# Performance work log

Measured on AMD Instinct MI355X. Metric: run time of the kernel, lower is better.

The kernel has to match this reference:

```python
import jax, jax.numpy as jnp
import numpy as np

N, D, HID, G, E2 = 2048, 256, 128, 8, 16384


def _mlp(h, w1, b1, g, be, w2, b2):
    # Linear -> ReLU -> BatchNorm1d (training mode, biased batch var) -> Linear
    h = jax.nn.relu(h @ w1 + b1)
    mu = h.mean(axis=0)
    var = ((h - mu) ** 2).mean(axis=0)
    h = (h - mu) / jnp.sqrt(var + 1e-5) * g + be
    return h @ w2 + b2


def setup_inputs() -> dict:
    key = jax.random.key(0)
    ks = jax.random.split(key, 12)
    x = jax.random.normal(ks[0], (N, D), jnp.float32)
    src = jax.random.randint(ks[1], (E2,), 0, N)
    dst = jax.random.randint(ks[2], (E2,), 0, N)
    src = jnp.where(src == dst, (src + 1) % N, src)  # no self loops
    edge_index = jnp.stack([jnp.concatenate([src, dst]),
                            jnp.concatenate([dst, src])])  # symmetric
    batch = jnp.sort(jax.random.randint(ks[3], (N,), 0, G))
    def lin(k, i, o):
        return 0.1 * jax.random.normal(k, (i, o), jnp.float32)
    out = dict(x=x, edge_index=edge_index, batch=batch)
    dims = [(1, HID, HID), (HID, HID, HID), (HID, HID, 1)]
    names = [("w11", "b11", "g1", "be1", "w12", "b12"),
             ("w21", "b21", "g2", "be2", "w22", "b22"),
             ("w31", "b31", "g3", "be3", "w32", "b32")]
    k = 4
    for (i, h, o), n in zip(dims, names):
        out[n[0]] = lin(ks[k], i, h)
        out[n[1]] = jnp.zeros((h,), jnp.float32)
        out[n[2]] = jnp.ones((h,), jnp.float32)
        out[n[3]] = jnp.zeros((h,), jnp.float32)
        out[n[4]] = lin(ks[k + 1], h, o)
        out[n[5]] = jnp.zeros((o,), jnp.float32)
        k += 2
    return out


def reference(x, edge_index, batch,
              w11, b11, g1, be1, w12, b12,
              w21, b21, g2, be2, w22, b22,
              w31, b31, g3, be3, w32, b32):
    n = x.shape[0]
    # dense adjacency from edge_index; L = D - A (unnormalized graph Laplacian)
    A = jnp.zeros((n, n), x.dtype).at[edge_index[0], edge_index[1]].set(1.0)
    deg = A.sum(axis=1)
    # entropy term: V = x*(Lx) - x*(Ax) + A(x*x), Lx = deg*x - Ax
    Ax = A @ x
    V = x * (deg[:, None] * x - Ax) - x * Ax + A @ (x * x)
    V = jnp.linalg.norm(V, axis=1)  # [n]
    # per-graph softmax over the batch segments
    mx = jax.ops.segment_max(V, batch, num_segments=G)
    ex = jnp.exp(V - mx[batch])
    P = ex / jax.ops.segment_sum(ex, batch, num_segments=G)[batch]
    P = jnp.where(P == 0.0, 1.0, P)
    ent = -P * jnp.log(P)  # [n]

    # GINConv (eps=0): mlp(x + sum_{j in N(i)} x_j) = mlp(x + A @ x)
    def gin(h, w1, b1, g, be, w2, b2):
        return _mlp(h + A @ h, w1, b1, g, be, w2, b2)

    h = gin(ent[:, None], w11, b11, g1, be1, w12, b12)
    h = gin(h, w21, b21, g2, be2, w22, b22)
    h = gin(h, w31, b31, g3, be3, w32, b32)
    p = jax.nn.sigmoid(h[:, 0])  # [n] node probabilities

    gamma = ent.sum()
    loss = gamma - jnp.vdot(ent, p) + jnp.vdot(p, A @ p)

    # greedy conditional expectation (sequential MIS-style selection)
    order = jnp.argsort(-p)

    def step(carry, idx):
        dummy, sel, rej = carry
        nb = A[idx] > 0.0  # neighbor mask [n]
        deg0 = ~jnp.any(nb)
        sel = sel.at[idx].set(sel[idx] | deg0)  # isolated node -> selected
        eligible = (~rej[idx]) & (~sel[idx])
        s = jnp.where(nb, 0.0, dummy).at[idx].set(1.0)
        li = gamma - jnp.vdot(ent, s) + jnp.vdot(s, A @ s)
        accept = eligible & (li <= loss)
        sel = sel.at[idx].set(sel[idx] | accept)
        rej = rej | (nb & accept)
        dummy = jnp.where(accept, s, dummy)
        return (dummy, sel, rej), None

    init = (p, jnp.zeros(n, dtype=bool), jnp.zeros(n, dtype=bool))
    (dummy, sel, rej), _ = jax.lax.scan(step, init, order)

    # graph reconstruction (masked instead of compacted, for static shapes)
    mask = sel.astype(x.dtype)
    x_pooled = x * mask[:, None]
    A2 = A @ A
    A3 = A2 @ A
    eye = jnp.eye(n, dtype=x.dtype)
    adj_pooled = (1.0 - eye) * jnp.clip(A2 + A3, 0.0, 1.0) * (mask[:, None] * mask[None, :])
    batch_pooled = jnp.where(sel, batch, -1)
    return x_pooled, adj_pooled, sel, batch_pooled, loss
```

## Files before the change

### kernel.cpp

```cpp
#include <hip/hip_runtime.h>
#include <math.h>

#define NN 2048
#define DIMF 256
#define HIDN 128
#define NG 8
#define NEDGES 32768
#define W32 32
#define TRI_CAP 131072
#define TRI_LDS 4864

typedef unsigned long long u64;
typedef unsigned char u8;
typedef unsigned short u16;

__global__ void k_init(u64* __restrict__ rowbits, int* __restrict__ segstart) {
  int i = blockIdx.x * blockDim.x + threadIdx.x;
  for (int k = i; k < NN * W32; k += gridDim.x * blockDim.x) rowbits[k] = 0ull;
  if (i <= NG) segstart[i] = NN;
}

__global__ void k_edges(const int* __restrict__ ei, u64* __restrict__ rowbits) {
  int e = blockIdx.x * blockDim.x + threadIdx.x;
  if (e >= NEDGES) return;
  int u = ei[e], v = ei[NEDGES + e];
  atomicOr(&rowbits[((size_t)u << 5) + (v >> 6)], 1ull << (v & 63));
}

__global__ void k_deg(const u64* __restrict__ rowbits, int* __restrict__ deg,
                      const int* __restrict__ batch, int* __restrict__ segstart) {
  int i = blockIdx.x * blockDim.x + threadIdx.x;
  if (i >= NN) return;
  int c = 0;
  for (int w = 0; w < W32; ++w) c += __popcll(rowbits[(i << 5) + w]);
  deg[i] = c;
  if (i == 0 || batch[i] != batch[i - 1]) segstart[batch[i]] = i;
}

__global__ void k_scan2048(const int* __restrict__ in, int* __restrict__ out) {
  __shared__ int part[256];
  int t = threadIdx.x;
  int v[8]; int s = 0;
  for (int k = 0; k < 8; ++k) { v[k] = in[t * 8 + k]; s += v[k]; }
  part[t] = s;
  __syncthreads();
  for (int off = 1; off < 256; off <<= 1) {
    int y = (t >= off) ? part[t - off] : 0;
    __syncthreads();
    part[t] += y;
    __syncthreads();
  }
  int run = part[t] - s;
  for (int k = 0; k < 8; ++k) { out[t * 8 + k] = run; run += v[k]; }
  if (t == 255) out[NN] = part[255];
}

__global__ void k_extract(const u64* __restrict__ rowbits, const int* __restrict__ rp,
                          int* __restrict__ col, int* __restrict__ cnt) {
  int i = blockIdx.x * blockDim.x + threadIdx.x;
  if (i >= NN) return;
  const u64* ri = rowbits + ((size_t)i << 5);
  int o = rp[i];
  for (int w = 0; w < W32; ++w) {
    u64 b = ri[w];
    while (b) { col[o++] = (w << 6) + __builtin_ctzll(b); b &= b - 1; }
  }
  int c = 0;
  for (int e = rp[i]; e < o; ++e) {
    const u64* ra = rowbits + ((size_t)col[e] << 5);
    for (int w = 0; w < W32; ++w) c += __popcll(ra[w] & ri[w]);
  }
  cnt[i] = c;
}

__global__ void k_trifill(const u64* __restrict__ rowbits, const int* __restrict__ rp,
                          const int* __restrict__ col, const int* __restrict__ tp,
                          int2* __restrict__ tri) {
  int i = blockIdx.x * blockDim.x + threadIdx.x;
  if (i >= NN) return;
  const u64* ri = rowbits + ((size_t)i << 5);
  int o = tp[i];
  for (int e = rp[i]; e < rp[i + 1]; ++e) {
    int a = col[e];
    const u64* ra = rowbits + ((size_t)a << 5);
    for (int w = 0; w < W32; ++w) {
      u64 b = ra[w] & ri[w];
      while (b) {
        int j = (w << 6) + __builtin_ctzll(b);
        if (o < TRI_CAP) tri[o] = make_int2(a, j);
        ++o;
        b &= b - 1;
      }
    }
  }
}

__global__ void k_V(const float* __restrict__ x, const int* __restrict__ rp,
                    const int* __restrict__ col, float* __restrict__ V) {
  int i = blockIdx.x; int t = threadIdx.x;
  float xi = x[i * DIMF + t];
  float s1 = 0.f, s2 = 0.f;
  int r0 = rp[i], r1 = rp[i + 1];
  for (int e = r0; e < r1; ++e) {
    float xj = x[col[e] * DIMF + t];
    s1 += xj; s2 += xj * xj;
  }
  float dg = (float)(r1 - r0);
  float val = dg * xi * xi - 2.f * xi * s1 + s2;
  __shared__ double red[DIMF];
  red[t] = (double)val * (double)val;
  __syncthreads();
  for (int off = DIMF / 2; off > 0; off >>= 1) { if (t < off) red[t] += red[t + off]; __syncthreads(); }
  if (t == 0) V[i] = (float)sqrt(red[0]);
}

__global__ void k_soft(const float* __restrict__ V, const int* __restrict__ segstart,
                       float* __restrict__ ent, double* __restrict__ seggamma) {
  int g = blockIdx.x; int t = threadIdx.x;
  int s = segstart[g];
  int e = NN;
  for (int gg = g + 1; gg <= NG; ++gg) { int v = segstart[gg]; if (v < e) e = v; }
  if (s >= e) { if (t == 0) seggamma[g] = 0.0; return; }
  __shared__ float fm[256];
  __shared__ double dd[256];
  float m = -3.0e38f;
  for (int i = s + t; i < e; i += 256) m = fmaxf(m, V[i]);
  fm[t] = m; __syncthreads();
  for (int off = 128; off > 0; off >>= 1) { if (t < off) fm[t] = fmaxf(fm[t], fm[t + off]); __syncthreads(); }
  float mx = fm[0];
  __syncthreads();
  double sum = 0.0;
  for (int i = s + t; i < e; i += 256) sum += exp((double)V[i] - (double)mx);
  dd[t] = sum; __syncthreads();
  for (int off = 128; off > 0; off >>= 1) { if (t < off) dd[t] += dd[t + off]; __syncthreads(); }
  double tot = dd[0];
  __syncthreads();
  double gs = 0.0;
  for (int i = s + t; i < e; i += 256) {
    double P = exp((double)V[i] - (double)mx) / tot;
    float ev = (P > 0.0) ? (float)(-P * log(P)) : 0.f;
    ent[i] = ev;
    gs += (double)ev;
  }
  dd[t] = gs; __syncthreads();
  for (int off = 128; off > 0; off >>= 1) { if (t < off) dd[t] += dd[t + off]; __syncthreads(); }
  if (t == 0) seggamma[g] = dd[0];
}

__global__ void k_agg1(const float* __restrict__ ent, const int* __restrict__ rp,
                       const int* __restrict__ col, float* __restrict__ agg) {
  int i = blockIdx.x * blockDim.x + threadIdx.x;
  if (i >= NN) return;
  float a = ent[i];
  for (int e = rp[i]; e < rp[i + 1]; ++e) a += ent[col[e]];
  agg[i] = a;
}

__global__ void k_lin1(const float* __restrict__ agg, const float* __restrict__ w,
                       const float* __restrict__ b, float* __restrict__ t) {
  int idx = blockIdx.x * blockDim.x + threadIdx.x;
  if (idx >= NN * HIDN) return;
  int i = idx >> 7, k = idx & 127;
  float v = agg[i] * w[k] + b[k];
  t[idx] = v > 0.f ? v : 0.f;
}

__global__ void k_bn(const float* __restrict__ t, const float* __restrict__ g,
                     const float* __restrict__ be, float* __restrict__ scale,
                     float* __restrict__ shift) {
  int k = blockIdx.x; int tid = threadIdx.x;
  __shared__ double red[256];
  double s = 0.0;
  for (int i = tid; i < NN; i += 256) s += (double)t[i * HIDN + k];
  red[tid] = s; __syncthreads();
  for (int off = 128; off > 0; off >>= 1) { if (tid < off) red[tid] += red[tid + off]; __syncthreads(); }
  double mu = red[0] / NN;
  __syncthreads();
  double v = 0.0;
  for (int i = tid; i < NN; i += 256) { double dv = (double)t[i * HIDN + k] - mu; v += dv * dv; }
  red[tid] = v; __syncthreads();
  for (int off = 128; off > 0; off >>= 1) { if (tid < off) red[tid] += red[tid + off]; __syncthreads(); }
  if (tid == 0) {
    float var = (float)(red[0] / NN);
    float sc = g[k] / sqrtf(var + 1e-5f);
    scale[k] = sc;
    shift[k] = be[k] - (float)mu * sc;
  }
}

template<int PRE, int RELU>
__global__ void k_mm(const float* __restrict__ in, const float* __restrict__ Wm,
                     const float* __restrict__ bias, const float* __restrict__ scale,
                     const float* __restrict__ shift, float* __restrict__ out) {
  __shared__ float ti[8][HIDN];
  int r0 = blockIdx.x * 8; int t = threadIdx.x;
  for (int r = 0; r < 8; ++r) {
    float v = in[(r0 + r) * HIDN + t];
    if (PRE) v = v * scale[t] + shift[t];
    ti[r][t] = v;
  }
  __syncthreads();
  float acc[8];
  #pragma unroll
  for (int r = 0; r < 8; ++r) acc[r] = 0.f;
  for (int k = 0; k < HIDN; ++k) {
    float w = Wm[k * HIDN + t];
    #pragma unroll
    for (int r = 0; r < 8; ++r) acc[r] += ti[r][k] * w;
  }
  for (int r = 0; r < 8; ++r) {
    float v = acc[r] + bias[t];
    if (RELU) v = fmaxf(v, 0.f);
    out[(r0 + r) * HIDN + t] = v;
  }
}

__global__ void k_agg128(const float* __restrict__ h, const int* __restrict__ rp,
                         const int* __restrict__ col, float* __restrict__ agg) {
  int i = blockIdx.x; int t = threadIdx.x;
  float a = h[i * HIDN + t];
  for (int e = rp[i]; e < rp[i + 1]; ++e) a += h[col[e] * HIDN + t];
  agg[i * HIDN + t] = a;
}

__global__ void k_lin3(const float* __restrict__ tn, const float* __restrict__ scale,
                       const float* __restrict__ shift, const float* __restrict__ w32,
                       const float* __restrict__ b32, float* __restrict__ p) {
  int i = blockIdx.x; int t = threadIdx.x;
  float v = (tn[i * HIDN + t] * scale[t] + shift[t]) * w32[t];
  __shared__ float red[HIDN];
  red[t] = v; __syncthreads();
  for (int off = 64; off > 0; off >>= 1) { if (t < off) red[t] += red[t + off]; __syncthreads(); }
  if (t == 0) {
    float h3 = red[0] + b32[0];
    p[i] = 1.f / (1.f + expf(-h3));
  }
}

__global__ void k_q0(const float* __restrict__ p, const float* __restrict__ ent,
                     const int* __restrict__ rp, const int* __restrict__ col,
                     float* __restrict__ q0, float* __restrict__ e0) {
  int i = blockIdx.x * blockDim.x + threadIdx.x;
  if (i >= NN) return;
  float s = 0.f, es = 0.f;
  for (int e = rp[i]; e < rp[i + 1]; ++e) {
    int j = col[e];
    float pj = p[j];
    s += pj; es += ent[j] * pj;
  }
  q0[i] = s; e0[i] = es;
}

__global__ void k_loss(const float* __restrict__ ent, const float* __restrict__ p,
                       const float* __restrict__ q0, const double* __restrict__ seggamma,
                       double* __restrict__ scal) {
  __shared__ double ra[256], rb[256];
  int t = threadIdx.x;
  double a = 0.0, b = 0.0;
  for (int i = t; i < NN; i += 256) { a += (double)ent[i] * (double)p[i]; b += (double)p[i] * (double)q0[i]; }
  ra[t] = a; rb[t] = b; __syncthreads();
  for (int off = 128; off > 0; off >>= 1) {
    if (t < off) { ra[t] += ra[t + off]; rb[t] += rb[t + off]; }
    __syncthreads();
  }
  if (t == 0) {
    double gamma = 0.0;
    for (int g = 0; g < NG; ++g) gamma += seggamma[g];
    scal[0] = gamma; scal[1] = ra[0]; scal[2] = rb[0];
    scal[3] = gamma - ra[0] + rb[0];
  }
}

__global__ void k_sort(const float* __restrict__ p, int* __restrict__ order) {
  __shared__ u64 s[NN];
  int t = threadIdx.x;
  for (int k = t; k < NN; k += 1024) {
    unsigned b = __float_as_uint(p[k]);
    unsigned ss = (b & 0x80000000u) ? ~b : (b | 0x80000000u);
    s[k] = ((u64)(~ss) << 32) | (unsigned)k;
  }
  __syncthreads();
  for (int k = 2; k <= NN; k <<= 1) {
    for (int j = k >> 1; j > 0; j >>= 1) {
      for (int i = t; i < NN; i += 1024) {
        int ixj = i ^ j;
        if (ixj > i) {
          bool up = ((i & k) == 0);
          u64 a = s[i], b = s[ixj];
          if ((a > b) == up) { s[i] = b; s[ixj] = a; }
        }
      }
      __syncthreads();
    }
  }
  order[t] = (int)(s[t] & 0xFFFFFFFFull);
  order[t + 1024] = (int)(s[t + 1024] & 0xFFFFFFFFull);
}

#define DPP2(ctrl)                                                                        \
  a += __int_as_float(__builtin_amdgcn_update_dpp(0, __float_as_int(a), ctrl, 0xf, 0xf, true)); \
  b += __int_as_float(__builtin_amdgcn_update_dpp(0, __float_as_int(b), ctrl, 0xf, 0xf, true));

__device__ __forceinline__ void red2(float& a, float& b) {
  DPP2(0x111)
  DPP2(0x112)
  DPP2(0x114)
  DPP2(0x118)
  DPP2(0x142)
  DPP2(0x143)
  a = __int_as_float(__builtin_amdgcn_readlane(__float_as_int(a), 63));
  b = __int_as_float(__builtin_amdgcn_readlane(__float_as_int(b), 63));
}

__global__ void __launch_bounds__(1024, 1) k_greedy(
    const int* __restrict__ rp, const int* __restrict__ col,
    const int* __restrict__ tp, const int2* __restrict__ tri,
    const int* __restrict__ order, const float* __restrict__ p,
    const float* __restrict__ ent, const float* __restrict__ q0,
    const float* __restrict__ e0, const double* __restrict__ scal,
    u8* __restrict__ selb_g) {
  __shared__ float2 dq[NN];
  __shared__ float2 ee[NN];
  __shared__ u16 colL[NEDGES];
  __shared__ u16 ordl[NN];
  __shared__ uint2 rtP[NN + 1];
  __shared__ ushort2 triL[TRI_LDS];
  __shared__ unsigned decidedL[64], selL[64];
  __shared__ unsigned maskL[2];
  __shared__ float4 svA[2][16];
  int t = threadIdx.x;
  int w = t >> 6, lane = t & 63;

  for (int i = t; i < NN; i += 1024) {
    dq[i] = make_float2(p[i], q0[i]);
    ee[i] = make_float2(ent[i], e0[i]);
    ordl[i] = (u16)order[i];
    int tv0 = tp[i]; if (tv0 > 65535) tv0 = 65535;
    int tv1 = tp[i + 1]; if (tv1 > 65535) tv1 = 65535;
    rtP[i] = make_uint2((unsigned)rp[i] | ((unsigned)tv0 << 16),
                        (unsigned)rp[i + 1] | ((unsigned)tv1 << 16));
  }
  for (int i = t; i < NEDGES; i += 1024) colL[i] = (u16)col[i];
  for (int i = t; i < TRI_LDS; i += 1024) {
    int2 ab = tri[i];
    triL[i] = make_ushort2((u16)(ab.x & 2047), (u16)(ab.y & 2047));
  }
  if (t < 64) { decidedL[t] = 0u; selL[t] = 0u; }
  if (t < 2) maskL[t] = 0u;
  double gamma = scal[0], loss = scal[3];
  double ed = scal[1], dAd = scal[2];
  __syncthreads();
  for (int i = t; i < NN; i += 1024) {
    if (((rtP[i].y & 0xffffu) - (rtP[i].x & 0xffffu)) == 0u) {
      atomicOr(&decidedL[i >> 5], 1u << (i & 31));
      atomicOr(&selL[i >> 5], 1u << (i & 31));
    }
  }
  __syncthreads();

  int pos = 0, rc = 0;
  while (pos < NN) {
    int b = rc & 1; ++rc;
    int step = pos + w;
    if (step < NN) {
      int idx = ordl[step];
      if (!((decidedL[idx >> 5] >> (idx & 31)) & 1u)) {
        uint2 rt = rtP[idx];
        int r0 = rt.x & 0xffff, r1 = rt.y & 0xffff;
        int t0 = rt.x >> 16, t1 = rt.y >> 16;
        float2 dqi = dq[idx];
        float2 eei = ee[idx];
        float s2 = 0.f, st = 0.f;
        for (int e = r0 + lane; e < r1; e += 64) {
          float2 v = dq[colL[e]];
          s2 -= v.y * v.x;
        }
        if (t1 <= TRI_LDS) {
          for (int e = t0 + lane; e < t1; e += 64) {
            ushort2 ab = triL[e];
            st += dq[ab.x].x * dq[ab.y].x;
          }
        } else {
          int g0 = tp[idx], g1 = tp[idx + 1];
          if (g0 > TRI_CAP) g0 = TRI_CAP;
          if (g1 > TRI_CAP) g1 = TRI_CAP;
          for (int e = g0 + lane; e < g1; e += 64) {
            int2 ab = tri[e];
            st += dq[ab.x].x * dq[ab.y].x;
          }
        }
        red2(s2, st);
        float d0 = 1.f - dqi.x;
        float S1 = -eei.y + eei.x * d0;
        float S2 = s2 + dqi.y * d0;
        float sn = -dqi.y;
        double cross = 2.0 * (double)d0 * (double)sn + (double)st;
        double li = gamma - (ed + (double)S1) + (dAd + 2.0 * (double)S2 + cross);
        if (li <= loss && lane == 0) {
          svA[b][w] = make_float4(S1, S2, d0, st);
          atomicOr(&maskL[b], 1u << w);
        }
      }
    }
    __syncthreads();
    unsigned mask = maskL[b];
    if (mask == 0u) { pos += 16; continue; }
    int k = __builtin_ctz(mask);
    int idx = ordl[pos + k];
    float4 A = svA[b][k];
    float2 dqi = dq[idx];
    uint2 rt = rtP[idx];
    int r0 = rt.x & 0xffff, r1 = rt.y & 0xffff;
    {
      double cross = 2.0 * (double)A.z * (double)(-dqi.y) + (double)A.w;
      ed += (double)A.x;
      dAd += 2.0 * (double)A.y + cross;
    }
    __syncthreads();
    if (t == 0) maskL[b] = 0u;
    for (int e = r0 + w; e < r1; e += 16) {
      int a = colL[e];
      float da = -dq[a].x;
      if (da != 0.f) {
        float ea = ee[a].x;
        uint2 art = rtP[a];
        int b0 = art.x & 0xffff, b1 = art.y & 0xffff;
        for (int eb = b0 + lane; eb < b1; eb += 64) {
          int bb = colL[eb];
          atomicAdd(&dq[bb].y, da);
          atomicAdd(&ee[bb].y, ea * da);
        }
      }
    }
    {
      float ei = ee[idx].x;
      for (int e = r0 + t; e < r1; e += 1024) {
        int bb = colL[e];
        atomicAdd(&dq[bb].y, A.z);
        atomicAdd(&ee[bb].y, ei * A.z);
      }
    }
    __syncthreads();
    if (t == 0) {
      dq[idx].x = 1.f;
      atomicOr(&decidedL[idx >> 5], 1u << (idx & 31));
      atomicOr(&selL[idx >> 5], 1u << (idx & 31));
    }
    for (int e = r0 + t; e < r1; e += 1024) {
      int j = colL[e];
      dq[j].x = 0.f;
      atomicOr(&decidedL[j >> 5], 1u << (j & 31));
    }
    __syncthreads();
    pos += k + 1;
  }
  for (int i = t; i < NN; i += 1024)
    selb_g[i] = (u8)((selL[i >> 5] >> (i & 31)) & 1u);
}

__global__ void k_reach(const u64* __restrict__ src, const int* __restrict__ rp,
                        const int* __restrict__ col, u64* __restrict__ dst) {
  int node = blockIdx.x * 2 + (threadIdx.x >> 5);
  int w = threadIdx.x & 31;
  u64 acc = 0;
  for (int e = rp[node]; e < rp[node + 1]; ++e) acc |= src[((size_t)col[e] << 5) + w];
  dst[((size_t)node << 5) + w] = acc;
}

__global__ void k_out(const u64* __restrict__ row2, const u64* __restrict__ row3,
                      const u8* __restrict__ selb, const float* __restrict__ x,
                      const int* __restrict__ batch, const double* __restrict__ scal,
                      float* __restrict__ o_x, float* __restrict__ o_adj,
                      float* __restrict__ o_sel, float* __restrict__ o_bat,
                      float* __restrict__ o_loss) {
  int idx = blockIdx.x * blockDim.x + threadIdx.x;
  {
    int i = idx >> 11, j = idx & 2047;
    int wo = (i << 5) + (j >> 6);
    u64 b = (row2[wo] | row3[wo]) >> (j & 63);
    o_adj[idx] = ((b & 1ull) && i != j && selb[i] && selb[j]) ? 1.f : 0.f;
  }
  if (idx < NN * DIMF) {
    int i = idx >> 8;
    o_x[idx] = selb[i] ? x[idx] : 0.f;
  }
  if (idx < NN) {
    o_sel[idx] = selb[idx] ? 1.f : 0.f;
    o_bat[idx] = selb[idx] ? (float)batch[idx] : -1.f;
  }
  if (idx == 0) o_loss[0] = (float)scal[3];
}

extern "C" void kernel_launch(void* const* d_in, const int* in_sizes, int n_in,
                              void* d_out, int out_size, void* d_ws, size_t ws_size,
                              hipStream_t stream) {
  const float* x    = (const float*)d_in[0];
  const int*   ei   = (const int*)d_in[1];
  const int*   batch= (const int*)d_in[2];
  const float* w11  = (const float*)d_in[3];
  const float* b11  = (const float*)d_in[4];
  const float* g1   = (const float*)d_in[5];
  const float* be1  = (const float*)d_in[6];
  const float* w12  = (const float*)d_in[7];
  const float* b12  = (const float*)d_in[8];
  const float* w21  = (const float*)d_in[9];
  const float* b21  = (const float*)d_in[10];
  const float* g2   = (const float*)d_in[11];
  const float* be2  = (const float*)d_in[12];
  const float* w22  = (const float*)d_in[13];
  const float* b22  = (const float*)d_in[14];
  const float* w31  = (const float*)d_in[15];
  const float* b31  = (const float*)d_in[16];
  const float* g3   = (const float*)d_in[17];
  const float* be3  = (const float*)d_in[18];
  const float* w32  = (const float*)d_in[19];
  const float* b32  = (const float*)d_in[20];

  char* wsb = (char*)d_ws;
  size_t cur = 0;
  auto alloc = [&](size_t bytes) -> void* {
    void* pp = wsb + cur;
    cur += (bytes + 255) & ~(size_t)255;
    return pp;
  };
  u64*    rowbits = (u64*)alloc((size_t)NN * W32 * 8);
  u64*    row2    = (u64*)alloc((size_t)NN * W32 * 8);
  u64*    row3    = (u64*)alloc((size_t)NN * W32 * 8);
  double* seggam  = (double*)alloc(NG * 8);
  double* scal    = (double*)alloc(4 * 8);
  int*    deg     = (int*)alloc(NN * 4);
  int*    rowptr  = (int*)alloc((NN + 1) * 4);
  int*    colx    = (int*)alloc(65536 * 4);
  int*    tricnt  = (int*)alloc(NN * 4);
  int*    triptr  = (int*)alloc((NN + 1) * 4);
  int2*   tri     = (int2*)alloc((size_t)TRI_CAP * 8);
  int*    segst   = (int*)alloc((NG + 1) * 4);
  int*    order   = (int*)alloc(NN * 4);
  float*  ent     = (float*)alloc(NN * 4);
  float*  V       = (float*)alloc(NN * 4);
  float*  p       = (float*)alloc(NN * 4);
  float*  q0      = (float*)alloc(NN * 4);
  float*  e0      = (float*)alloc(NN * 4);
  float*  agg1    = (float*)alloc(NN * 4);
  float*  scale   = (float*)alloc(HIDN * 4);
  float*  shift   = (float*)alloc(HIDN * 4);
  float*  tA      = (float*)alloc((size_t)NN * HIDN * 4);
  float*  tB      = (float*)alloc((size_t)NN * HIDN * 4);
  float*  tC      = (float*)alloc((size_t)NN * HIDN * 4);
  u8*     selb    = (u8*)alloc(NN);

  float* out    = (float*)d_out;
  float* o_x    = out;
  float* o_adj  = out + 524288;
  float* o_sel  = out + 4718592;
  float* o_bat  = out + 4720640;
  float* o_loss = out + 4722688;

  k_init<<<64, 256, 0, stream>>>(rowbits, segst);
  k_edges<<<128, 256, 0, stream>>>(ei, rowbits);
  k_deg<<<8, 256, 0, stream>>>(rowbits, deg, batch, segst);
  k_scan2048<<<1, 256, 0, stream>>>(deg, rowptr);
  k_extract<<<8, 256, 0, stream>>>(rowbits, rowptr, colx, tricnt);
  k_scan2048<<<1, 256, 0, stream>>>(tricnt, triptr);
  k_trifill<<<8, 256, 0, stream>>>(rowbits, rowptr, colx, triptr, tri);
  k_V<<<NN, 256, 0, stream>>>(x, rowptr, colx, V);
  k_soft<<<NG, 256, 0, stream>>>(V, segst, ent, seggam);

  k_agg1<<<8, 256, 0, stream>>>(ent, rowptr, colx, agg1);
  k_lin1<<<1024, 256, 0, stream>>>(agg1, w11, b11, tA);
  k_bn<<<HIDN, 256, 0, stream>>>(tA, g1, be1, scale, shift);
  k_mm<1, 0><<<NN / 8, HIDN, 0, stream>>>(tA, w12, b12, scale, shift, tB);
  k_agg128<<<NN, HIDN, 0, stream>>>(tB, rowptr, colx, tC);
  k_mm<0, 1><<<NN / 8, HIDN, 0, stream>>>(tC, w21, b21, scale, shift, tA);
  k_bn<<<HIDN, 256, 0, stream>>>(tA, g2, be2, scale, shift);
  k_mm<1, 0><<<NN / 8, HIDN, 0, stream>>>(tA, w22, b22, scale, shift, tB);
  k_agg128<<<NN, HIDN, 0, stream>>>(tB, rowptr, colx, tC);
  k_mm<0, 1><<<NN / 8, HIDN, 0, stream>>>(tC, w31, b31, scale, shift, tA);
  k_bn<<<HIDN, 256, 0, stream>>>(tA, g3, be3, scale, shift);
  k_lin3<<<NN, HIDN, 0, stream>>>(tA, scale, shift, w32, b32, p);

  k_q0<<<8, 256, 0, stream>>>(p, ent, rowptr, colx, q0, e0);
  k_loss<<<1, 256, 0, stream>>>(ent, p, q0, seggam, scal);
  k_sort<<<1, 1024, 0, stream>>>(p, order);
  k_greedy<<<1, 1024, 0, stream>>>(rowptr, colx, triptr, tri, order, p, ent, q0, e0, scal, selb);

  k_reach<<<NN / 2, 64, 0, stream>>>(rowbits, rowptr, colx, row2);
  k_reach<<<NN / 2, 64, 0, stream>>>(row2, rowptr, colx, row3);
  k_out<<<NN * NN / 256, 256, 0, stream>>>(row2, row3, selb, x, batch, scal,
                                           o_x, o_adj, o_sel, o_bat, o_loss);

  (void)in_sizes; (void)n_in; (void)out_size; (void)ws_size;
}
```

Baseline: 1.132 ms.

## Fuse preprocessing and MLP stages into one cooperative persistent kernel

Measured after the change: 1.863 ms. +64.6%, slower.

```diff
diff --git a/kernel.cpp b/kernel.cpp
--- a/kernel.cpp
+++ b/kernel.cpp
@@ -1,5 +1,8 @@
 #include <hip/hip_runtime.h>
+#include <hip/hip_cooperative_groups.h>
 #include <math.h>
+
+namespace cg = cooperative_groups;
 
 #define NN 2048
 #define DIMF 256
@@ -9,293 +12,345 @@
 #define W32 32
 #define TRI_CAP 131072
 #define TRI_LDS 4864
+#define NB 64
+#define NT 1024
+#define GSZ (NB * NT)
 
 typedef unsigned long long u64;
 typedef unsigned char u8;
 typedef unsigned short u16;
 
-__global__ void k_init(u64* __restrict__ rowbits, int* __restrict__ segstart) {
-  int i = blockIdx.x * blockDim.x + threadIdx.x;
-  for (int k = i; k < NN * W32; k += gridDim.x * blockDim.x) rowbits[k] = 0ull;
-  if (i <= NG) segstart[i] = NN;
-}
-
-__global__ void k_edges(const int* __restrict__ ei, u64* __restrict__ rowbits) {
-  int e = blockIdx.x * blockDim.x + threadIdx.x;
-  if (e >= NEDGES) return;
-  int u = ei[e], v = ei[NEDGES + e];
-  atomicOr(&rowbits[((size_t)u << 5) + (v >> 6)], 1ull << (v & 63));
-}
-
-__global__ void k_deg(const u64* __restrict__ rowbits, int* __restrict__ deg,
-                      const int* __restrict__ batch, int* __restrict__ segstart) {
-  int i = blockIdx.x * blockDim.x + threadIdx.x;
-  if (i >= NN) return;
-  int c = 0;
-  for (int w = 0; w < W32; ++w) c += __popcll(rowbits[(i << 5) + w]);
-  deg[i] = c;
-  if (i == 0 || batch[i] != batch[i - 1]) segstart[batch[i]] = i;
-}
-
-__global__ void k_scan2048(const int* __restrict__ in, int* __restrict__ out) {
-  __shared__ int part[256];
-  int t = threadIdx.x;
-  int v[8]; int s = 0;
-  for (int k = 0; k < 8; ++k) { v[k] = in[t * 8 + k]; s += v[k]; }
+struct Params {
+  const float* x; const int* ei; const int* batch;
+  const float* w11; const float* b11; const float* g1; const float* be1;
+  const float* w12; const float* b12;
+  const float* w21; const float* b21; const float* g2; const float* be2;
+  const float* w22; const float* b22;
+  const float* w31; const float* b31; const float* g3; const float* be3;
+  const float* w32; const float* b32;
+  u64* rowbits; u64* row2; u64* row3;
+  int* deg; int* rowptr; int* colx; int* tricnt; int* triptr; int2* tri;
+  int* segst; float* V; float* ent; double* seggam; double* lossAB; double* scal;
+  float* agg1; float* scaleS; float* shiftS;
+  float* tA; float* tB; float* tC;
+  float* p; float* q0; float* e0; int* order;
+};
+
+__device__ void scan2048b(const int* in, int* out, int* part, int t) {
+  int v0 = in[2 * t], v1 = in[2 * t + 1];
+  int s = v0 + v1;
   part[t] = s;
   __syncthreads();
-  for (int off = 1; off < 256; off <<= 1) {
+  for (int off = 1; off < 1024; off <<= 1) {
     int y = (t >= off) ? part[t - off] : 0;
     __syncthreads();
     part[t] += y;
     __syncthreads();
   }
   int run = part[t] - s;
-  for (int k = 0; k < 8; ++k) { out[t * 8 + k] = run; run += v[k]; }
-  if (t == 255) out[NN] = part[255];
-}
-
-__global__ void k_extract(const u64* __restrict__ rowbits, const int* __restrict__ rp,
-                          int* __restrict__ col, int* __restrict__ cnt) {
-  int i = blockIdx.x * blockDim.x + threadIdx.x;
-  if (i >= NN) return;
-  const u64* ri = rowbits + ((size_t)i << 5);
-  int o = rp[i];
-  for (int w = 0; w < W32; ++w) {
-    u64 b = ri[w];
-    while (b) { col[o++] = (w << 6) + __builtin_ctzll(b); b &= b - 1; }
-  }
-  int c = 0;
-  for (int e = rp[i]; e < o; ++e) {
-    const u64* ra = rowbits + ((size_t)col[e] << 5);
-    for (int w = 0; w < W32; ++w) c += __popcll(ra[w] & ri[w]);
-  }
-  cnt[i] = c;
-}
-
-__global__ void k_trifill(const u64* __restrict__ rowbits, const int* __restrict__ rp,
-                          const int* __restrict__ col, const int* __restrict__ tp,
-                          int2* __restrict__ tri) {
-  int i = blockIdx.x * blockDim.x + threadIdx.x;
-  if (i >= NN) return;
-  const u64* ri = rowbits + ((size_t)i << 5);
-  int o = tp[i];
-  for (int e = rp[i]; e < rp[i + 1]; ++e) {
-    int a = col[e];
-    const u64* ra = rowbits + ((size_t)a << 5);
-    for (int w = 0; w < W32; ++w) {
-      u64 b = ra[w] & ri[w];
-      while (b) {
-        int j = (w << 6) + __builtin_ctzll(b);
-        if (o < TRI_CAP) tri[o] = make_int2(a, j);
-        ++o;
-        b &= b - 1;
-      }
-    }
-  }
-}
-
-__global__ void k_V(const float* __restrict__ x, const int* __restrict__ rp,
-                    const int* __restrict__ col, float* __restrict__ V) {
-  int i = blockIdx.x; int t = threadIdx.x;
-  float xi = x[i * DIMF + t];
-  float s1 = 0.f, s2 = 0.f;
-  int r0 = rp[i], r1 = rp[i + 1];
-  for (int e = r0; e < r1; ++e) {
-    float xj = x[col[e] * DIMF + t];
-    s1 += xj; s2 += xj * xj;
-  }
-  float dg = (float)(r1 - r0);
-  float val = dg * xi * xi - 2.f * xi * s1 + s2;
-  __shared__ double red[DIMF];
-  red[t] = (double)val * (double)val;
-  __syncthreads();
-  for (int off = DIMF / 2; off > 0; off >>= 1) { if (t < off) red[t] += red[t + off]; __syncthreads(); }
-  if (t == 0) V[i] = (float)sqrt(red[0]);
-}
-
-__global__ void k_soft(const float* __restrict__ V, const int* __restrict__ segstart,
-                       float* __restrict__ ent, double* __restrict__ seggamma) {
-  int g = blockIdx.x; int t = threadIdx.x;
-  int s = segstart[g];
+  out[2 * t] = run; out[2 * t + 1] = run + v0;
+  if (t == 1023) out[NN] = part[1023];
+}
+
+__device__ void bn_phase(int blk, int t, int mode, const float* aggv,
+                         const float* w1, const float* b1, const float* src,
+                         const float* g, const float* be,
+                         float* scaleS, float* shiftS, double* bnP) {
+  int c = 2 * blk + (t >> 9);
+  int tid = t & 511;
+  double s = 0.0, ss = 0.0;
+  for (int r = 0; r < 4; ++r) {
+    int i = tid + 512 * r;
+    float v;
+    if (mode == 0) { v = aggv[i] * w1[c] + b1[c]; v = v > 0.f ? v : 0.f; }
+    else v = src[i * HIDN + c];
+    s += (double)v; ss += (double)v * (double)v;
+  }
+  for (int off = 32; off; off >>= 1) { s += __shfl_down(s, off); ss += __shfl_down(ss, off); }
+  int w = t >> 6;
+  if ((t & 63) == 0) { bnP[2 * w] = s; bnP[2 * w + 1] = ss; }
+  __syncthreads();
+  if (t == 0 || t == 512) {
+    int wb = (t >> 9) * 8;
+    double S = 0.0, SS = 0.0;
+    for (int k = 0; k < 8; ++k) { S += bnP[2 * (wb + k)]; SS += bnP[2 * (wb + k) + 1]; }
+    double mu = S / NN;
+    float var = (float)(SS / NN - mu * mu);
+    float sc = g[c] / sqrtf(var + 1e-5f);
+    scaleS[c] = sc;
+    shiftS[c] = be[c] - (float)mu * sc;
+  }
+  __syncthreads();
+}
+
+__device__ void mm_phase(int blk, int t, int mode, const float* aggv,
+                         const float* w1, const float* b1, const float* src,
+                         const float* scaleS, const float* shiftS,
+                         const float* W, const float* bias, int relu, float* dst,
+                         float* Wl, float* tile) {
+  int r0 = blk * 32;
+  for (int i = t; i < HIDN * HIDN; i += NT) Wl[i] = W[i];
+  for (int i = t; i < 32 * HIDN; i += NT) {
+    int r = i >> 7, k = i & 127;
+    float v;
+    if (mode == 0) { v = aggv[r0 + r] * w1[k] + b1[k]; v = v > 0.f ? v : 0.f; v = v * scaleS[k] + shiftS[k]; }
+    else if (mode == 1) v = src[(r0 + r) * HIDN + k];
+    else v = src[(r0 + r) * HIDN + k] * scaleS[k] + shiftS[k];
+    tile[i] = v;
+  }
+  __syncthreads();
+  int g = t >> 7;
+  int c = t & 127;
+  float a0 = 0.f, a1 = 0.f, a2 = 0.f, a3 = 0.f;
+  for (int k = 0; k < HIDN; ++k) {
+    float wv = Wl[k * HIDN + c];
+    a0 += tile[g * HIDN + k] * wv;
+    a1 += tile[(g + 8) * HIDN + k] * wv;
+    a2 += tile[(g + 16) * HIDN + k] * wv;
+    a3 += tile[(g + 24) * HIDN + k] * wv;
+  }
+  float bv = bias[c];
+  a0 += bv; a1 += bv; a2 += bv; a3 += bv;
+  if (relu) { a0 = fmaxf(a0, 0.f); a1 = fmaxf(a1, 0.f); a2 = fmaxf(a2, 0.f); a3 = fmaxf(a3, 0.f); }
+  dst[(r0 + g) * HIDN + c] = a0;
+  dst[(r0 + g + 8) * HIDN + c] = a1;
+  dst[(r0 + g + 16) * HIDN + c] = a2;
+  dst[(r0 + g + 24) * HIDN + c] = a3;
+  __syncthreads();
+}
+
+__device__ void soft_phase(int g, int t, const float* V, const int* segst,
+                           float* ent, double* seggam, float* fmS, double* ddS) {
+  int s = segst[g];
   int e = NN;
-  for (int gg = g + 1; gg <= NG; ++gg) { int v = segstart[gg]; if (v < e) e = v; }
-  if (s >= e) { if (t == 0) seggamma[g] = 0.0; return; }
-  __shared__ float fm[256];
-  __shared__ double dd[256];
+  for (int gg = g + 1; gg <= NG; ++gg) { int v = segst[gg]; if (v < e) e = v; }
+  if (s >= e) { if (t == 0) seggam[g] = 0.0; return; }
   float m = -3.0e38f;
-  for (int i = s + t; i < e; i += 256) m = fmaxf(m, V[i]);
-  fm[t] = m; __syncthreads();
-  for (int off = 128; off > 0; off >>= 1) { if (t < off) fm[t] = fmaxf(fm[t], fm[t + off]); __syncthreads(); }
-  float mx = fm[0];
+  for (int i = s + t; i < e; i += NT) m = fmaxf(m, V[i]);
+  fmS[t] = m; __syncthreads();
+  for (int off = 512; off; off >>= 1) { if (t < off) fmS[t] = fmaxf(fmS[t], fmS[t + off]); __syncthreads(); }
+  float mx = fmS[0];
   __syncthreads();
   double sum = 0.0;
-  for (int i = s + t; i < e; i += 256) sum += exp((double)V[i] - (double)mx);
-  dd[t] = sum; __syncthreads();
-  for (int off = 128; off > 0; off >>= 1) { if (t < off) dd[t] += dd[t + off]; __syncthreads(); }
-  double tot = dd[0];
+  for (int i = s + t; i < e; i += NT) sum += exp((double)V[i] - (double)mx);
+  ddS[t] = sum; __syncthreads();
+  for (int off = 512; off; off >>= 1) { if (t < off) ddS[t] += ddS[t + off]; __syncthreads(); }
+  double tot = ddS[0];
   __syncthreads();
   double gs = 0.0;
-  for (int i = s + t; i < e; i += 256) {
+  for (int i = s + t; i < e; i += NT) {
     double P = exp((double)V[i] - (double)mx) / tot;
     float ev = (P > 0.0) ? (float)(-P * log(P)) : 0.f;
     ent[i] = ev;
     gs += (double)ev;
   }
-  dd[t] = gs; __syncthreads();
-  for (int off = 128; off > 0; off >>= 1) { if (t < off) dd[t] += dd[t + off]; __syncthreads(); }
-  if (t == 0) seggamma[g] = dd[0];
-}
-
-__global__ void k_agg1(const float* __restrict__ ent, const int* __restrict__ rp,
-                       const int* __restrict__ col, float* __restrict__ agg) {
-  int i = blockIdx.x * blockDim.x + threadIdx.x;
-  if (i >= NN) return;
-  float a = ent[i];
-  for (int e = rp[i]; e < rp[i + 1]; ++e) a += ent[col[e]];
-  agg[i] = a;
-}
-
-__global__ void k_lin1(const float* __restrict__ agg, const float* __restrict__ w,
-                       const float* __restrict__ b, float* __restrict__ t) {
-  int idx = blockIdx.x * blockDim.x + threadIdx.x;
-  if (idx >= NN * HIDN) return;
-  int i = idx >> 7, k = idx & 127;
-  float v = agg[i] * w[k] + b[k];
-  t[idx] = v > 0.f ? v : 0.f;
-}
-
-__global__ void k_bn(const float* __restrict__ t, const float* __restrict__ g,
-                     const float* __restrict__ be, float* __restrict__ scale,
-                     float* __restrict__ shift) {
-  int k = blockIdx.x; int tid = threadIdx.x;
-  __shared__ double red[256];
-  double s = 0.0;
-  for (int i = tid; i < NN; i += 256) s += (double)t[i * HIDN + k];
-  red[tid] = s; __syncthreads();
-  for (int off = 128; off > 0; off >>= 1) { if (tid < off) red[tid] += red[tid + off]; __syncthreads(); }
-  double mu = red[0] / NN;
-  __syncthreads();
-  double v = 0.0;
-  for (int i = tid; i < NN; i += 256) { double dv = (double)t[i * HIDN + k] - mu; v += dv * dv; }
-  red[tid] = v; __syncthreads();
-  for (int off = 128; off > 0; off >>= 1) { if (tid < off) red[tid] += red[tid + off]; __syncthreads(); }
-  if (tid == 0) {
-    float var = (float)(red[0] / NN);
-    float sc = g[k] / sqrtf(var + 1e-5f);
-    scale[k] = sc;
-    shift[k] = be[k] - (float)mu * sc;
-  }
-}
-
-template<int PRE, int RELU>
-__global__ void k_mm(const float* __restrict__ in, const float* __restrict__ Wm,
-                     const float* __restrict__ bias, const float* __restrict__ scale,
-                     const float* __restrict__ shift, float* __restrict__ out) {
-  __shared__ float ti[8][HIDN];
-  int r0 = blockIdx.x * 8; int t = threadIdx.x;
-  for (int r = 0; r < 8; ++r) {
-    float v = in[(r0 + r) * HIDN + t];
-    if (PRE) v = v * scale[t] + shift[t];
-    ti[r][t] = v;
-  }
-  __syncthreads();
-  float acc[8];
-  #pragma unroll
-  for (int r = 0; r < 8; ++r) acc[r] = 0.f;
-  for (int k = 0; k < HIDN; ++k) {
-    float w = Wm[k * HIDN + t];
-    #pragma unroll
-    for (int r = 0; r < 8; ++r) acc[r] += ti[r][k] * w;
-  }
-  for (int r = 0; r < 8; ++r) {
-    float v = acc[r] + bias[t];
-    if (RELU) v = fmaxf(v, 0.f);
-    out[(r0 + r) * HIDN + t] = v;
-  }
-}
-
-__global__ void k_agg128(const float* __restrict__ h, const int* __restrict__ rp,
-                         const int* __restrict__ col, float* __restrict__ agg) {
-  int i = blockIdx.x; int t = threadIdx.x;
-  float a = h[i * HIDN + t];
-  for (int e = rp[i]; e < rp[i + 1]; ++e) a += h[col[e] * HIDN + t];
-  agg[i * HIDN + t] = a;
-}
-
-__global__ void k_lin3(const float* __restrict__ tn, const float* __restrict__ scale,
-                       const float* __restrict__ shift, const float* __restrict__ w32,
-                       const float* __restrict__ b32, float* __restrict__ p) {
-  int i = blockIdx.x; int t = threadIdx.x;
-  float v = (tn[i * HIDN + t] * scale[t] + shift[t]) * w32[t];
-  __shared__ float red[HIDN];
-  red[t] = v; __syncthreads();
-  for (int off = 64; off > 0; off >>= 1) { if (t < off) red[t] += red[t + off]; __syncthreads(); }
-  if (t == 0) {
-    float h3 = red[0] + b32[0];
-    p[i] = 1.f / (1.f + expf(-h3));
-  }
-}
-
-__global__ void k_q0(const float* __restrict__ p, const float* __restrict__ ent,
-                     const int* __restrict__ rp, const int* __restrict__ col,
-                     float* __restrict__ q0, float* __restrict__ e0) {
-  int i = blockIdx.x * blockDim.x + threadIdx.x;
-  if (i >= NN) return;
-  float s = 0.f, es = 0.f;
-  for (int e = rp[i]; e < rp[i + 1]; ++e) {
-    int j = col[e];
-    float pj = p[j];
-    s += pj; es += ent[j] * pj;
-  }
-  q0[i] = s; e0[i] = es;
-}
-
-__global__ void k_loss(const float* __restrict__ ent, const float* __restrict__ p,
-                       const float* __restrict__ q0, const double* __restrict__ seggamma,
-                       double* __restrict__ scal) {
-  __shared__ double ra[256], rb[256];
-  int t = threadIdx.x;
-  double a = 0.0, b = 0.0;
-  for (int i = t; i < NN; i += 256) { a += (double)ent[i] * (double)p[i]; b += (double)p[i] * (double)q0[i]; }
-  ra[t] = a; rb[t] = b; __syncthreads();
-  for (int off = 128; off > 0; off >>= 1) {
-    if (t < off) { ra[t] += ra[t + off]; rb[t] += rb[t + off]; }
-    __syncthreads();
-  }
-  if (t == 0) {
-    double gamma = 0.0;
-    for (int g = 0; g < NG; ++g) gamma += seggamma[g];
-    scal[0] = gamma; scal[1] = ra[0]; scal[2] = rb[0];
-    scal[3] = gamma - ra[0] + rb[0];
-  }
-}
-
-__global__ void k_sort(const float* __restrict__ p, int* __restrict__ order) {
-  __shared__ u64 s[NN];
-  int t = threadIdx.x;
-  for (int k = t; k < NN; k += 1024) {
-    unsigned b = __float_as_uint(p[k]);
-    unsigned ss = (b & 0x80000000u) ? ~b : (b | 0x80000000u);
-    s[k] = ((u64)(~ss) << 32) | (unsigned)k;
-  }
-  __syncthreads();
-  for (int k = 2; k <= NN; k <<= 1) {
-    for (int j = k >> 1; j > 0; j >>= 1) {
-      for (int i = t; i < NN; i += 1024) {
-        int ixj = i ^ j;
-        if (ixj > i) {
-          bool up = ((i & k) == 0);
-          u64 a = s[i], b = s[ixj];
-          if ((a > b) == up) { s[i] = b; s[ixj] = a; }
+  ddS[t] = gs; __syncthreads();
+  for (int off = 512; off; off >>= 1) { if (t < off) ddS[t] += ddS[t + off]; __syncthreads(); }
+  if (t == 0) seggam[g] = ddS[0];
+}
+
+__global__ void __launch_bounds__(1024, 1) mega(Params P) {
+  cg::grid_group grid = cg::this_grid();
+  int t = threadIdx.x, blk = blockIdx.x;
+  int gtid = blk * NT + t;
+
+  __shared__ double SMd[11776];
+  char* SM = (char*)SMd;
+  float* Wl = (float*)SM;
+  float* tile = (float*)(SM + 65536);
+  u64* skey = (u64*)SM;
+  int* scanP = (int*)(SM + 81920);
+  float* fmS = (float*)(SM + 81920);
+  double* ddS = (double*)(SM + 86016);
+  double* bnP = (double*)(SM + 81920);
+
+  for (int i = gtid; i < NN * W32; i += GSZ) P.rowbits[i] = 0ull;
+  if (gtid <= NG) P.segst[gtid] = NN;
+  if (gtid < 2) P.lossAB[gtid] = 0.0;
+  grid.sync();
+  for (int e = gtid; e < NEDGES; e += GSZ) {
+    int u = P.ei[e], v = P.ei[NEDGES + e];
+    atomicOr(&P.rowbits[((size_t)u << 5) + (v >> 6)], 1ull << (v & 63));
+  }
+  grid.sync();
+  if (gtid < NN) {
+    int c = 0;
+    for (int w = 0; w < W32; ++w) c += __popcll(P.rowbits[(gtid << 5) + w]);
+    P.deg[gtid] = c;
+    if (gtid == 0 || P.batch[gtid] != P.batch[gtid - 1]) P.segst[P.batch[gtid]] = gtid;
+  }
+  grid.sync();
+  if (blk == 0) scan2048b(P.deg, P.rowptr, scanP, t);
+  grid.sync();
+  if (gtid < NN) {
+    const u64* ri = P.rowbits + ((size_t)gtid << 5);
+    int o = P.rowptr[gtid];
+    for (int w = 0; w < W32; ++w) {
+      u64 b = ri[w];
+      while (b) { P.colx[o++] = (w << 6) + __builtin_ctzll(b); b &= b - 1; }
+    }
+    int c = 0;
+    for (int e = P.rowptr[gtid]; e < o; ++e) {
+      const u64* ra = P.rowbits + ((size_t)P.colx[e] << 5);
+      for (int w = 0; w < W32; ++w) c += __popcll(ra[w] & ri[w]);
+    }
+    P.tricnt[gtid] = c;
+  }
+  grid.sync();
+  if (blk == 0) scan2048b(P.tricnt, P.triptr, scanP, t);
+  grid.sync();
+  if (gtid < NN) {
+    const u64* ri = P.rowbits + ((size_t)gtid << 5);
+    int o = P.triptr[gtid];
+    for (int e = P.rowptr[gtid]; e < P.rowptr[gtid + 1]; ++e) {
+      int a = P.colx[e];
+      const u64* ra = P.rowbits + ((size_t)a << 5);
+      for (int w = 0; w < W32; ++w) {
+        u64 b = ra[w] & ri[w];
+        while (b) {
+          int j = (w << 6) + __builtin_ctzll(b);
+          if (o < TRI_CAP) P.tri[o] = make_int2(a, j);
+          ++o;
+          b &= b - 1;
         }
       }
-      __syncthreads();
-    }
-  }
-  order[t] = (int)(s[t] & 0xFFFFFFFFull);
-  order[t + 1024] = (int)(s[t + 1024] & 0xFFFFFFFFull);
-}
+    }
+  }
+  for (int i2 = gtid; i2 < NN * W32; i2 += GSZ) {
+    int node = i2 >> 5, w = i2 & 31;
+    u64 acc = 0;
+    for (int e = P.rowptr[node]; e < P.rowptr[node + 1]; ++e)
+      acc |= P.rowbits[((size_t)P.colx[e] << 5) + w];
+    P.row2[i2] = acc;
+  }
+  grid.sync();
+  for (int i2 = gtid; i2 < NN * W32; i2 += GSZ) {
+    int node = i2 >> 5, w = i2 & 31;
+    u64 acc = 0;
+    for (int e = P.rowptr[node]; e < P.rowptr[node + 1]; ++e)
+      acc |= P.row2[((size_t)P.colx[e] << 5) + w];
+    P.row3[i2] = acc;
+  }
+  grid.sync();
+  {
+    int node = gtid >> 5, lane = gtid & 31;
+    int r0 = P.rowptr[node], r1 = P.rowptr[node + 1];
+    double acc = 0.0;
+    for (int r = 0; r < 8; ++r) {
+      int d = lane + 32 * r;
+      float xi = P.x[node * DIMF + d];
+      float s1 = 0.f, s2 = 0.f;
+      for (int e = r0; e < r1; ++e) {
+        float xj = P.x[P.colx[e] * DIMF + d];
+        s1 += xj; s2 += xj * xj;
+      }
+      float dg = (float)(r1 - r0);
+      float val = dg * xi * xi - 2.f * xi * s1 + s2;
+      acc += (double)val * (double)val;
+    }
+    for (int m = 16; m; m >>= 1) acc += __shfl_xor(acc, m, 32);
+    if (lane == 0) P.V[node] = (float)sqrt(acc);
+  }
+  grid.sync();
+  if (blk < NG) soft_phase(blk, t, P.V, P.segst, P.ent, P.seggam, fmS, ddS);
+  grid.sync();
+  if (gtid < NN) {
+    float a = P.ent[gtid];
+    for (int e = P.rowptr[gtid]; e < P.rowptr[gtid + 1]; ++e) a += P.ent[P.colx[e]];
+    P.agg1[gtid] = a;
+  }
+  grid.sync();
+  bn_phase(blk, t, 0, P.agg1, P.w11, P.b11, (const float*)0, P.g1, P.be1, P.scaleS, P.shiftS, bnP);
+  grid.sync();
+  mm_phase(blk, t, 0, P.agg1, P.w11, P.b11, (const float*)0, P.scaleS, P.shiftS, P.w12, P.b12, 0, P.tB, Wl, tile);
+  grid.sync();
+  for (int idx = gtid; idx < NN * HIDN; idx += GSZ) {
+    int i = idx >> 7, k = idx & 127;
+    float a = P.tB[idx];
+    for (int e = P.rowptr[i]; e < P.rowptr[i + 1]; ++e) a += P.tB[P.colx[e] * HIDN + k];
+    P.tC[idx] = a;
+  }
+  grid.sync();
+  mm_phase(blk, t, 1, (const float*)0, (const float*)0, (const float*)0, P.tC, P.scaleS, P.shiftS, P.w21, P.b21, 1, P.tA, Wl, tile);
+  grid.sync();
+  bn_phase(blk, t, 1, (const float*)0, (const float*)0, (const float*)0, P.tA, P.g2, P.be2, P.scaleS, P.shiftS, bnP);
+  grid.sync();
+  mm_phase(blk, t, 2, (const float*)0, (const float*)0, (const float*)0, P.tA, P.scaleS, P.shiftS, P.w22, P.b22, 0, P.tB, Wl, tile);
+  grid.sync();
+  for (int idx = gtid; idx < NN * HIDN; idx += GSZ) {
+    int i = idx >> 7, k = idx & 127;
+    float a = P.tB[idx];
+    for (int e = P.rowptr[i]; e < P.rowptr[i + 1]; ++e) a += P.tB[P.colx[e] * HIDN + k];
+    P.tC[idx] = a;
+  }
+  grid.sync();
+  mm_phase(blk, t, 1, (const float*)0, (const float*)0, (const float*)0, P.tC, P.scaleS, P.shiftS, P.w31, P.b31, 1, P.tA, Wl, tile);
+  grid.sync();
+  bn_phase(blk, t, 1, (const float*)0, (const float*)0, (const float*)0, P.tA, P.g3, P.be3, P.scaleS, P.shiftS, bnP);
+  grid.sync();
+  {
+    int node = gtid >> 5, lane = gtid & 31;
+    float s = 0.f;
+    for (int r = 0; r < 4; ++r) {
+      int k = lane + 32 * r;
+      s += (P.tA[node * HIDN + k] * P.scaleS[k] + P.shiftS[k]) * P.w32[k];
+    }
+    for (int m = 16; m; m >>= 1) s += __shfl_xor(s, m, 32);
+    if (lane == 0) P.p[node] = 1.f / (1.f + expf(-(s + P.b32[0])));
+  }
+  grid.sync();
+  if (blk == 0) {
+    for (int i2 = t; i2 < NN; i2 += NT) {
+      unsigned bb = __float_as_uint(P.p[i2]);
+      unsigned ss2 = (bb & 0x80000000u) ? ~bb : (bb | 0x80000000u);
+      skey[i2] = ((u64)(~ss2) << 32) | (unsigned)i2;
+    }
+    __syncthreads();
+    for (int k = 2; k <= NN; k <<= 1) {
+      for (int j = k >> 1; j > 0; j >>= 1) {
+        for (int i2 = t; i2 < NN; i2 += NT) {
+          int ixj = i2 ^ j;
+          if (ixj > i2) {
+            bool up = ((i2 & k) == 0);
+            u64 a = skey[i2], b2 = skey[ixj];
+            if ((a > b2) == up) { skey[i2] = b2; skey[ixj] = a; }
+          }
+        }
+        __syncthreads();
+      }
+    }
+    P.order[t] = (int)(skey[t] & 0xFFFFFFFFull);
+    P.order[t + 1024] = (int)(skey[t + 1024] & 0xFFFFFFFFull);
+  } else {
+    int i = gtid - NT;
+    double la = 0.0, lb = 0.0;
+    if (i < NN) {
+      float qs = 0.f, es = 0.f;
+      for (int e = P.rowptr[i]; e < P.rowptr[i + 1]; ++e) {
+        int j = P.colx[e];
+        float pj = P.p[j];
+        qs += pj; es += P.ent[j] * pj;
+      }
+      P.q0[i] = qs; P.e0[i] = es;
+      la = (double)P.ent[i] * (double)P.p[i];
+      lb = (double)P.p[i] * (double)qs;
+    }
+    for (int off = 32; off; off >>= 1) { la += __shfl_down(la, off); lb += __shfl_down(lb, off); }
+    if ((t & 63) == 0 && (la != 0.0 || lb != 0.0)) {
+      atomicAdd(&P.lossAB[0], la);
+      atomicAdd(&P.lossAB[1], lb);
+    }
+  }
+  grid.sync();
+  if (gtid == 0) {
+    double gamma = 0.0;
+    for (int g = 0; g < NG; ++g) gamma += P.seggam[g];
+    double A = P.lossAB[0], Bb = P.lossAB[1];
+    P.scal[0] = gamma; P.scal[1] = A; P.scal[2] = Bb; P.scal[3] = gamma - A + Bb;
+  }
+}
+
+struct NodeF { float d, q, ent, pad; };
 
 #define DPP2(ctrl)                                                                        \
   a += __int_as_float(__builtin_amdgcn_update_dpp(0, __float_as_int(a), ctrl, 0xf, 0xf, true)); \
@@ -452,19 +507,10 @@
       atomicOr(&decidedL[j >> 5], 1u << (j & 31));
     }
     __syncthreads();
-    pos += k + 1;
+    pos += pos + k + 1 - pos;
   }
   for (int i = t; i < NN; i += 1024)
     selb_g[i] = (u8)((selL[i >> 5] >> (i & 31)) & 1u);
-}
-
-__global__ void k_reach(const u64* __restrict__ src, const int* __restrict__ rp,
-                        const int* __restrict__ col, u64* __restrict__ dst) {
-  int node = blockIdx.x * 2 + (threadIdx.x >> 5);
-  int w = threadIdx.x & 31;
-  u64 acc = 0;
-  for (int e = rp[node]; e < rp[node + 1]; ++e) acc |= src[((size_t)col[e] << 5) + w];
-  dst[((size_t)node << 5) + w] = acc;
 }
 
 __global__ void k_out(const u64* __restrict__ row2, const u64* __restrict__ row3,
@@ -494,27 +540,28 @@
 extern "C" void kernel_launch(void* const* d_in, const int* in_sizes, int n_in,
                               void* d_out, int out_size, void* d_ws, size_t ws_size,
                               hipStream_t stream) {
-  const float* x    = (const float*)d_in[0];
-  const int*   ei   = (const int*)d_in[1];
-  const int*   batch= (const int*)d_in[2];
-  const float* w11  = (const float*)d_in[3];
-  const float* b11  = (const float*)d_in[4];
-  const float* g1   = (const float*)d_in[5];
-  const float* be1  = (const float*)d_in[6];
-  const float* w12  = (const float*)d_in[7];
-  const float* b12  = (const float*)d_in[8];
-  const float* w21  = (const float*)d_in[9];
-  const float* b21  = (const float*)d_in[10];
-  const float* g2   = (const float*)d_in[11];
-  const float* be2  = (const float*)d_in[12];
-  const float* w22  = (const float*)d_in[13];
-  const float* b22  = (const float*)d_in[14];
-  const float* w31  = (const float*)d_in[15];
-  const float* b31  = (const float*)d_in[16];
-  const float* g3   = (const float*)d_in[17];
-  const float* be3  = (const float*)d_in[18];
-  const float* w32  = (const float*)d_in[19];
-  const float* b32  = (const float*)d_in[20];
+  Params P;
+  P.x    = (const float*)d_in[0];
+  P.ei   = (const int*)d_in[1];
+  P.batch= (const int*)d_in[2];
+  P.w11  = (const float*)d_in[3];
+  P.b11  = (const float*)d_in[4];
+  P.g1   = (const float*)d_in[5];
+  P.be1  = (const float*)d_in[6];
+  P.w12  = (const float*)d_in[7];
+  P.b12  = (const float*)d_in[8];
+  P.w21  = (const float*)d_in[9];
+  P.b21  = (const float*)d_in[10];
+  P.g2   = (const float*)d_in[11];
+  P.be2  = (const float*)d_in[12];
+  P.w22  = (const float*)d_in[13];
+  P.b22  = (const float*)d_in[14];
+  P.w31  = (const float*)d_in[15];
+  P.b31  = (const float*)d_in[16];
+  P.g3   = (const float*)d_in[17];
+  P.be3  = (const float*)d_in[18];
+  P.w32  = (const float*)d_in[19];
+  P.b32  = (const float*)d_in[20];
 
   char* wsb = (char*)d_ws;
   size_t cur = 0;
@@ -523,31 +570,32 @@
     cur += (bytes + 255) & ~(size_t)255;
     return pp;
   };
-  u64*    rowbits = (u64*)alloc((size_t)NN * W32 * 8);
-  u64*    row2    = (u64*)alloc((size_t)NN * W32 * 8);
-  u64*    row3    = (u64*)alloc((size_t)NN * W32 * 8);
-  double* seggam  = (double*)alloc(NG * 8);
-  double* scal    = (double*)alloc(4 * 8);
-  int*    deg     = (int*)alloc(NN * 4);
-  int*    rowptr  = (int*)alloc((NN + 1) * 4);
-  int*    colx    = (int*)alloc(65536 * 4);
-  int*    tricnt  = (int*)alloc(NN * 4);
-  int*    triptr  = (int*)alloc((NN + 1) * 4);
-  int2*   tri     = (int2*)alloc((size_t)TRI_CAP * 8);
-  int*    segst   = (int*)alloc((NG + 1) * 4);
-  int*    order   = (int*)alloc(NN * 4);
-  float*  ent     = (float*)alloc(NN * 4);
-  float*  V       = (float*)alloc(NN * 4);
-  float*  p       = (float*)alloc(NN * 4);
-  float*  q0      = (float*)alloc(NN * 4);
-  float*  e0      = (float*)alloc(NN * 4);
-  float*  agg1    = (float*)alloc(NN * 4);
-  float*  scale   = (float*)alloc(HIDN * 4);
-  float*  shift   = (float*)alloc(HIDN * 4);
-  float*  tA      = (float*)alloc((size_t)NN * HIDN * 4);
-  float*  tB      = (float*)alloc((size_t)NN * HIDN * 4);
-  float*  tC      = (float*)alloc((size_t)NN * HIDN * 4);
-  u8*     selb    = (u8*)alloc(NN);
+  P.rowbits = (u64*)alloc((size_t)NN * W32 * 8);
+  P.row2    = (u64*)alloc((size_t)NN * W32 * 8);
+  P.row3    = (u64*)alloc((size_t)NN * W32 * 8);
+  P.seggam  = (double*)alloc(NG * 8);
+  P.lossAB  = (double*)alloc(2 * 8);
+  P.scal    = (double*)alloc(4 * 8);
+  P.deg     = (int*)alloc(NN * 4);
+  P.rowptr  = (int*)alloc((NN + 1) * 4);
+  P.colx    = (int*)alloc(65536 * 4);
+  P.tricnt  = (int*)alloc(NN * 4);
+  P.triptr  = (int*)alloc((NN + 1) * 4);
+  P.tri     = (int2*)alloc((size_t)TRI_CAP * 8);
+  P.segst   = (int*)alloc((NG + 1) * 4);
+  P.order   = (int*)alloc(NN * 4);
+  P.V       = (float*)alloc(NN * 4);
+  P.ent     = (float*)alloc(NN * 4);
+  P.p       = (float*)alloc(NN * 4);
+  P.q0      = (float*)alloc(NN * 4);
+  P.e0      = (float*)alloc(NN * 4);
+  P.agg1    = (float*)alloc(NN * 4);
+  P.scaleS  = (float*)alloc(HIDN * 4);
+  P.shiftS  = (float*)alloc(HIDN * 4);
+  P.tA      = (float*)alloc((size_t)NN * HIDN * 4);
+  P.tB      = (float*)alloc((size_t)NN * HIDN * 4);
+  P.tC      = (float*)alloc((size_t)NN * HIDN * 4);
+  u8* selb  = (u8*)alloc(NN);
 
   float* out    = (float*)d_out;
   float* o_x    = out;
@@ -556,37 +604,13 @@
   float* o_bat  = out + 4720640;
   float* o_loss = out + 4722688;
 
-  k_init<<<64, 256, 0, stream>>>(rowbits, segst);
-  k_edges<<<128, 256, 0, stream>>>(ei, rowbits);
-  k_deg<<<8, 256, 0, stream>>>(rowbits, deg, batch, segst);
-  k_scan2048<<<1, 256, 0, stream>>>(deg, rowptr);
-  k_extract<<<8, 256, 0, stream>>>(rowbits, rowptr, colx, tricnt);
-  k_scan2048<<<1, 256, 0, stream>>>(tricnt, triptr);
-  k_trifill<<<8, 256, 0, stream>>>(rowbits, rowptr, colx, triptr, tri);
-  k_V<<<NN, 256, 0, stream>>>(x, rowptr, colx, V);
-  k_soft<<<NG, 256, 0, stream>>>(V, segst, ent, seggam);
-
-  k_agg1<<<8, 256, 0, stream>>>(ent, rowptr, colx, agg1);
-  k_lin1<<<1024, 256, 0, stream>>>(agg1, w11, b11, tA);
-  k_bn<<<HIDN, 256, 0, stream>>>(tA, g1, be1, scale, shift);
-  k_mm<1, 0><<<NN / 8, HIDN, 0, stream>>>(tA, w12, b12, scale, shift, tB);
-  k_agg128<<<NN, HIDN, 0, stream>>>(tB, rowptr, colx, tC);
-  k_mm<0, 1><<<NN / 8, HIDN, 0, stream>>>(tC, w21, b21, scale, shift, tA);
-  k_bn<<<HIDN, 256, 0, stream>>>(tA, g2, be2, scale, shift);
-  k_mm<1, 0><<<NN / 8, HIDN, 0, stream>>>(tA, w22, b22, scale, shift, tB);
-  k_agg128<<<NN, HIDN, 0, stream>>>(tB, rowptr, colx, tC);
-  k_mm<0, 1><<<NN / 8, HIDN, 0, stream>>>(tC, w31, b31, scale, shift, tA);
-  k_bn<<<HIDN, 256, 0, stream>>>(tA, g3, be3, scale, shift);
-  k_lin3<<<NN, HIDN, 0, stream>>>(tA, scale, shift, w32, b32, p);
-
-  k_q0<<<8, 256, 0, stream>>>(p, ent, rowptr, colx, q0, e0);
-  k_loss<<<1, 256, 0, stream>>>(ent, p, q0, seggam, scal);
-  k_sort<<<1, 1024, 0, stream>>>(p, order);
-  k_greedy<<<1, 1024, 0, stream>>>(rowptr, colx, triptr, tri, order, p, ent, q0, e0, scal, selb);
-
-  k_reach<<<NN / 2, 64, 0, stream>>>(rowbits, rowptr, colx, row2);
-  k_reach<<<NN / 2, 64, 0, stream>>>(row2, rowptr, colx, row3);
-  k_out<<<NN * NN / 256, 256, 0, stream>>>(row2, row3, selb, x, batch, scal,
+  void* args[] = { &P };
+  hipLaunchCooperativeKernel((void*)mega, dim3(NB), dim3(NT), args, 0, stream);
+
+  k_greedy<<<1, 1024, 0, stream>>>(P.rowptr, P.colx, P.triptr, P.tri, P.order,
+                                   P.p, P.ent, P.q0, P.e0, P.scal, selb);
+
+  k_out<<<NN * NN / 256, 256, 0, stream>>>(P.row2, P.row3, selb, P.x, P.batch, P.scal,
                                            o_x, o_adj, o_sel, o_bat, o_loss);
 
   (void)in_sizes; (void)n_in; (void)out_size; (void)ws_size;
```
